# Performance work log

Measured on AMD Instinct MI355X. Metric: run time of the kernel, lower is better.

## Reference

```python
import jax, jax.numpy as jnp
import numpy as np

D_MODEL, NUM_HEADS, D_HEAD = 1024, 16, 64
B, T = 2, 2048


def setup_inputs() -> dict:
    key = jax.random.key(0)
    ks = jax.random.split(key, 9)
    s_in = 1.0 / np.sqrt(D_MODEL)
    s_proj = 1.0 / np.sqrt(NUM_HEADS * D_HEAD)
    x = jax.random.normal(ks[0], (B, T, D_MODEL), dtype=jnp.float32)
    # stacked per-head projection weights (nn.Linear: y = x @ W.T + b -> store as [H, C, d_head])
    Wq = jax.random.uniform(ks[1], (NUM_HEADS, D_MODEL, D_HEAD), jnp.float32, -s_in, s_in)
    Wk = jax.random.uniform(ks[2], (NUM_HEADS, D_MODEL, D_HEAD), jnp.float32, -s_in, s_in)
    Wv = jax.random.uniform(ks[3], (NUM_HEADS, D_MODEL, D_HEAD), jnp.float32, -s_in, s_in)
    bq = jax.random.uniform(ks[4], (NUM_HEADS, D_HEAD), jnp.float32, -s_in, s_in)
    bk = jax.random.uniform(ks[5], (NUM_HEADS, D_HEAD), jnp.float32, -s_in, s_in)
    bv = jax.random.uniform(ks[6], (NUM_HEADS, D_HEAD), jnp.float32, -s_in, s_in)
    Wo = jax.random.uniform(ks[7], (NUM_HEADS * D_HEAD, D_MODEL), jnp.float32, -s_proj, s_proj)
    bo = jax.random.uniform(ks[8], (D_MODEL,), jnp.float32, -s_proj, s_proj)
    return {"x": x, "Wq": Wq, "Wk": Wk, "Wv": Wv, "bq": bq, "bk": bk, "bv": bv, "Wo": Wo, "bo": bo}


def reference(x, Wq, Wk, Wv, bq, bk, bv, Wo, bo):
    Bsz, Tlen, C = x.shape
    # per-head projections, vectorized over heads: [B, H, T, d_head]
    q = jnp.einsum('btc,hcd->bhtd', x, Wq) + bq[None, :, None, :]
    k = jnp.einsum('btc,hcd->bhtd', x, Wk) + bk[None, :, None, :]
    v = jnp.einsum('btc,hcd->bhtd', x, Wv) + bv[None, :, None, :]
    # NOTE: source scales by sqrt(C) = sqrt(d_model), not sqrt(d_head); no causal mask
    scores = jnp.einsum('bhtd,bhsd->bhts', q, k) / jnp.sqrt(jnp.asarray(C, x.dtype))
    attn = jax.nn.softmax(scores, axis=-1)
    out = jnp.einsum('bhts,bhsd->bhtd', attn, v)  # [B, H, T, d_head]
    # concat heads along feature dim: [B, T, H*d_head]
    out = jnp.transpose(out, (0, 2, 1, 3)).reshape(Bsz, Tlen, -1)
    return out @ Wo + bo
```

## Files before the change

kernel.cpp:

```cpp
#include <hip/hip_runtime.h>

typedef __bf16 bf16;
typedef __bf16 bf16x4 __attribute__((ext_vector_type(4)));
typedef __bf16 bf16x8 __attribute__((ext_vector_type(8)));
typedef float  f32x4  __attribute__((ext_vector_type(4)));

#define T_SEQ  2048
#define NHEAD  16
#define DHEAD  64
#define DMODEL 1024
#define MTOT   4096
#define L2E    1.4426950408889634f

static __device__ __forceinline__ f32x4 mfma16(bf16x8 a, bf16x8 b, f32x4 c) {
    return __builtin_amdgcn_mfma_f32_16x16x32_bf16(a, b, c, 0, 0, 0);
}

__global__ __launch_bounds__(256) void prep(
    const float* __restrict__ x,  bf16* __restrict__ xbf,
    const float* __restrict__ Wq, const float* __restrict__ Wk,
    const float* __restrict__ Wv, bf16* __restrict__ wt,
    const float* __restrict__ Wo, bf16* __restrict__ wot)
{
    __shared__ float t[64][68];
    const int bid = blockIdx.x, tid = threadIdx.x;

    if (bid < 2048) {
        const int i = bid * 256 + tid;
        const float4 a = ((const float4*)x)[i * 2];
        const float4 b = ((const float4*)x)[i * 2 + 1];
        bf16x8 v;
        v[0] = (bf16)a.x; v[1] = (bf16)a.y; v[2] = (bf16)a.z; v[3] = (bf16)a.w;
        v[4] = (bf16)b.x; v[5] = (bf16)b.y; v[6] = (bf16)b.z; v[7] = (bf16)b.w;
        ((bf16x8*)xbf)[i] = v;
        return;
    }

    const float* in; bf16* out;
    int R, Cc; long ib, ob; int r0, c0;
    if (bid < 2816) {
        int b2 = bid - 2048;
        int w = b2 >> 8, rem = b2 & 255;
        int rt = rem & 15, head = rem >> 4;
        in  = (w == 0 ? Wq : w == 1 ? Wk : Wv);
        out = wt + (size_t)w * 1024 * 1024;
        R = 1024; Cc = 64;
        ib = (long)head * 65536; ob = (long)head * 65536;
        r0 = rt * 64; c0 = 0;
    } else {
        int b3 = bid - 2816;
        in = Wo; out = wot;
        R = 1024; Cc = 1024;
        ib = 0; ob = 0;
        r0 = (b3 & 15) * 64; c0 = (b3 >> 4) * 64;
    }

#pragma unroll
    for (int i = 0; i < 4; ++i) {
        int idx = i * 256 + tid;
        int row = idx >> 4, cb = (idx & 15) * 4;
        float4 v = *(const float4*)&in[ib + (long)(r0 + row) * Cc + c0 + cb];
        t[row][cb + 0] = v.x; t[row][cb + 1] = v.y;
        t[row][cb + 2] = v.z; t[row][cb + 3] = v.w;
    }
    __syncthreads();
#pragma unroll
    for (int i = 0; i < 2; ++i) {
        int idx = i * 256 + tid;
        int row = idx >> 3, cb = (idx & 7) * 8;
        bf16x8 v;
#pragma unroll
        for (int j = 0; j < 8; ++j) v[j] = (bf16)t[cb + j][row];
        *(bf16x8*)&out[ob + (long)(c0 + row) * R + r0 + cb] = v;
    }
}

__global__ __launch_bounds__(256) void qkv_gemm(
    const bf16* __restrict__ x, const bf16* __restrict__ wt,
    const float* __restrict__ bq, const float* __restrict__ bk,
    const float* __restrict__ bv,
    bf16* __restrict__ qws, bf16* __restrict__ kws, bf16* __restrict__ vtws)
{
    __shared__ __align__(16) bf16 xs[128][72];
    __shared__ __align__(16) bf16 wsh[3][64][72];

    const int m0 = blockIdx.x * 128;
    const int h  = blockIdx.y;
    const int tid = threadIdx.x, wid = tid >> 6, lane = tid & 63;
    const int lr = lane & 15, lg = lane >> 4;

    const bf16* wbase[3];
#pragma unroll
    for (int w = 0; w < 3; ++w)
        wbase[w] = wt + ((size_t)(w * NHEAD + h)) * DHEAD * DMODEL;

    f32x4 acc[3][2][4];
#pragma unroll
    for (int w = 0; w < 3; ++w)
#pragma unroll
        for (int mi = 0; mi < 2; ++mi)
#pragma unroll
            for (int nt = 0; nt < 4; ++nt) acc[w][mi][nt] = (f32x4)0.0f;

    bf16x8 xr[4], wr[3][2];
#pragma unroll
    for (int i = 0; i < 4; ++i) {
        int idx = i * 256 + tid;
        int row = idx >> 3, cb = (idx & 7) * 8;
        xr[i] = *(const bf16x8*)&x[(size_t)(m0 + row) * DMODEL + cb];
    }
#pragma unroll
    for (int w = 0; w < 3; ++w)
#pragma unroll
        for (int i = 0; i < 2; ++i) {
            int idx = i * 256 + tid;
            int row = idx >> 3, cb = (idx & 7) * 8;
            wr[w][i] = *(const bf16x8*)&wbase[w][(size_t)row * DMODEL + cb];
        }

    for (int kt = 0; kt < 16; ++kt) {
        __syncthreads();
#pragma unroll
        for (int i = 0; i < 4; ++i) {
            int idx = i * 256 + tid;
            int row = idx >> 3, cb = (idx & 7) * 8;
            *(bf16x8*)&xs[row][cb] = xr[i];
        }
#pragma unroll
        for (int w = 0; w < 3; ++w)
#pragma unroll
            for (int i = 0; i < 2; ++i) {
                int idx = i * 256 + tid;
                int row = idx >> 3, cb = (idx & 7) * 8;
                *(bf16x8*)&wsh[w][row][cb] = wr[w][i];
            }
        __syncthreads();

        if (kt < 15) {
            const int kofs = (kt + 1) * 64;
#pragma unroll
            for (int i = 0; i < 4; ++i) {
                int idx = i * 256 + tid;
                int row = idx >> 3, cb = (idx & 7) * 8;
                xr[i] = *(const bf16x8*)&x[(size_t)(m0 + row) * DMODEL + kofs + cb];
            }
#pragma unroll
            for (int w = 0; w < 3; ++w)
#pragma unroll
                for (int i = 0; i < 2; ++i) {
                    int idx = i * 256 + tid;
                    int row = idx >> 3, cb = (idx & 7) * 8;
                    wr[w][i] = *(const bf16x8*)&wbase[w][(size_t)row * DMODEL + kofs + cb];
                }
        }

        bf16x8 af[2][2];
#pragma unroll
        for (int mi = 0; mi < 2; ++mi)
#pragma unroll
            for (int ks = 0; ks < 2; ++ks)
                af[mi][ks] = *(const bf16x8*)&xs[wid * 32 + mi * 16 + lr][ks * 32 + lg * 8];

#pragma unroll
        for (int w = 0; w < 3; ++w)
#pragma unroll
            for (int nt = 0; nt < 4; ++nt)
#pragma unroll
                for (int ks = 0; ks < 2; ++ks) {
                    bf16x8 bfr = *(const bf16x8*)&wsh[w][nt * 16 + lr][ks * 32 + lg * 8];
#pragma unroll
                    for (int mi = 0; mi < 2; ++mi)
                        acc[w][mi][nt] = mfma16(af[mi][ks], bfr, acc[w][mi][nt]);
                }
    }

    const float* bias[3] = { bq + h * DHEAD, bk + h * DHEAD, bv + h * DHEAD };
#pragma unroll
    for (int w = 0; w < 3; ++w)
#pragma unroll
        for (int nt = 0; nt < 4; ++nt) {
            int d = nt * 16 + lr;
            float bs = bias[w][d];
#pragma unroll
            for (int mi = 0; mi < 2; ++mi)
#pragma unroll
                for (int j = 0; j < 4; ++j) {
                    int mrow = m0 + wid * 32 + mi * 16 + lg * 4 + j;
                    int b = mrow >> 11, t = mrow & 2047;
                    float val = acc[w][mi][nt][j] + bs;
                    size_t bh = (size_t)b * NHEAD + h;
                    if (w == 0)
                        qws[(bh * T_SEQ + t) * DHEAD + d] = (bf16)val;
                    else if (w == 1)
                        kws[(bh * T_SEQ + t) * DHEAD + d] = (bf16)val;
                    else
                        vtws[(bh * DHEAD + d) * T_SEQ + t] = (bf16)val;
                }
        }
}

template<int S, bool PARTIAL>
__global__ __launch_bounds__(512) void attn_split(
    const bf16* __restrict__ qws, const bf16* __restrict__ kws,
    const bf16* __restrict__ vtws,
    bf16* __restrict__ po, float* __restrict__ pml, bf16* __restrict__ aws)
{
    __shared__ __align__(16) bf16 kls[2][64][72];
    __shared__ __align__(16) bf16 vls[2][64][72];
    __shared__ __align__(16) bf16 pls[128][68];

    const int id = blockIdx.x;
    const int w  = (id & 7) * (64 * S) + (id >> 3);
    const int bh = w / (16 * S);
    const int rem = w - bh * (16 * S);
    const int qt = rem / S;
    const int sidx = rem - qt * S;
    const int t0 = (sidx * 32) / S, t1 = ((sidx + 1) * 32) / S;

    const int b = bh >> 4, h = bh & 15;
    const bf16* Q  = qws  + (size_t)bh * T_SEQ * DHEAD;
    const bf16* K  = kws  + (size_t)bh * T_SEQ * DHEAD;
    const bf16* Vt = vtws + (size_t)bh * DHEAD * T_SEQ;

    const int tid = threadIdx.x, wid = tid >> 6, lane = tid & 63;
    const int lr = lane & 15, lg = lane >> 4;
    const int q0 = qt * 128 + wid * 16;

    const int srow = tid >> 3, scb = (tid & 7) * 8;

    bf16x8 qf[2];
#pragma unroll
    for (int ks = 0; ks < 2; ++ks) {
        bf16x8 v = *(const bf16x8*)&Q[(size_t)(q0 + lr) * DHEAD + ks * 32 + lg * 8];
#pragma unroll
        for (int j = 0; j < 8; ++j) v[j] = (bf16)((float)v[j] * 0.03125f);
        qf[ks] = v;
    }

    f32x4 o[4];
#pragma unroll
    for (int nt = 0; nt < 4; ++nt) o[nt] = (f32x4)0.0f;
    float mrun = -1e30f, lrun = 0.f;

    bf16x8 kr, vr;
    kr = *(const bf16x8*)&K[(size_t)(t0 * 64 + srow) * DHEAD + scb];
    vr = *(const bf16x8*)&Vt[(size_t)srow * T_SEQ + t0 * 64 + scb];
    *(bf16x8*)&kls[0][srow][scb] = kr;
    *(bf16x8*)&vls[0][srow][scb] = vr;

    int cur = 0;
    for (int t = t0; t < t1; ++t) {
        __syncthreads();

        const bool more = (t + 1) < t1;
        if (more) {
            int kvn = (t + 1) * 64;
            kr = *(const bf16x8*)&K[(size_t)(kvn + srow) * DHEAD + scb];
            vr = *(const bf16x8*)&Vt[(size_t)srow * T_SEQ + kvn + scb];
        }

        f32x4 s[4];
        __builtin_amdgcn_s_setprio(1);
#pragma unroll
        for (int nt = 0; nt < 4; ++nt) {
            bf16x8 k0 = *(const bf16x8*)&kls[cur][nt * 16 + lr][0 + lg * 8];
            bf16x8 k1 = *(const bf16x8*)&kls[cur][nt * 16 + lr][32 + lg * 8];
            s[nt] = mfma16(k0, qf[0], (f32x4)0.0f);
            s[nt] = mfma16(k1, qf[1], s[nt]);
        }
        __builtin_amdgcn_s_setprio(0);

        float vm0 = fmaxf(fmaxf(s[0][0], s[0][1]), fmaxf(s[0][2], s[0][3]));
        float vm1 = fmaxf(fmaxf(s[1][0], s[1][1]), fmaxf(s[1][2], s[1][3]));
        float vm2 = fmaxf(fmaxf(s[2][0], s[2][1]), fmaxf(s[2][2], s[2][3]));
        float vm3 = fmaxf(fmaxf(s[3][0], s[3][1]), fmaxf(s[3][2], s[3][3]));
        float vm = fmaxf(fmaxf(vm0, vm1), fmaxf(vm2, vm3));
        vm = fmaxf(vm, __shfl_xor(vm, 16));
        vm = fmaxf(vm, __shfl_xor(vm, 32));

        const bool skip = __all(vm <= mrun + 8.0f);
        float mnew = skip ? mrun : fmaxf(mrun, vm);
        float m2 = mnew * L2E;

        float p[4][4];
        float rs = 0.f;
#pragma unroll
        for (int nt = 0; nt < 4; ++nt)
#pragma unroll
            for (int j = 0; j < 4; ++j) {
                p[nt][j] = __builtin_amdgcn_exp2f(fmaf(s[nt][j], L2E, -m2));
                rs += p[nt][j];
            }

        if (skip) {
            lrun += rs;
        } else {
            float alpha = __builtin_amdgcn_exp2f((mrun - mnew) * L2E);
            lrun = lrun * alpha + rs;
            mrun = mnew;
            float ab[4];
#pragma unroll
            for (int j = 0; j < 4; ++j) ab[j] = __shfl(alpha, lg * 4 + j);
#pragma unroll
            for (int nt = 0; nt < 4; ++nt)
#pragma unroll
                for (int j = 0; j < 4; ++j) o[nt][j] *= ab[j];
        }

#pragma unroll
        for (int nt = 0; nt < 4; ++nt) {
            bf16x4 pk;
            pk[0] = (bf16)p[nt][0]; pk[1] = (bf16)p[nt][1];
            pk[2] = (bf16)p[nt][2]; pk[3] = (bf16)p[nt][3];
            *(bf16x4*)&pls[wid * 16 + lr][nt * 16 + 4 * lg] = pk;
        }

        asm volatile("s_waitcnt lgkmcnt(0)" ::: "memory");

        __builtin_amdgcn_s_setprio(1);
#pragma unroll
        for (int ks = 0; ks < 2; ++ks) {
            bf16x4 ph0 = *(const bf16x4*)&pls[wid * 16 + lr][ks * 32 + lg * 8];
            bf16x4 ph1 = *(const bf16x4*)&pls[wid * 16 + lr][ks * 32 + lg * 8 + 4];
            bf16x8 pf = __builtin_shufflevector(ph0, ph1, 0, 1, 2, 3, 4, 5, 6, 7);
#pragma unroll
            for (int nt = 0; nt < 4; ++nt) {
                bf16x8 vf = *(const bf16x8*)&vls[cur][nt * 16 + lr][ks * 32 + lg * 8];
                o[nt] = mfma16(pf, vf, o[nt]);
            }
        }
        __builtin_amdgcn_s_setprio(0);

        if (more) {
            *(bf16x8*)&kls[cur ^ 1][srow][scb] = kr;
            *(bf16x8*)&vls[cur ^ 1][srow][scb] = vr;
        }
        cur ^= 1;
    }

    float lrow = lrun;
    lrow += __shfl_xor(lrow, 16);
    lrow += __shfl_xor(lrow, 32);

    float linv[4];
#pragma unroll
    for (int j = 0; j < 4; ++j) linv[j] = 1.0f / __shfl(lrow, lg * 4 + j);

    if (PARTIAL) {
        const size_t pbase = (size_t)(sidx * 32 + bh) * T_SEQ * DHEAD;
#pragma unroll
        for (int nt = 0; nt < 4; ++nt) {
            int d = nt * 16 + lr;
#pragma unroll
            for (int j = 0; j < 4; ++j) {
                int tq = q0 + lg * 4 + j;
                po[pbase + (size_t)tq * DHEAD + d] = (bf16)(o[nt][j] * linv[j]);
            }
        }
        if (lg == 0) {
            size_t mlidx = ((size_t)(sidx * 32 + bh) * T_SEQ + (q0 + lr)) * 2;
            pml[mlidx]     = mrun;
            pml[mlidx + 1] = lrow;
        }
    } else {
        const size_t obase = ((size_t)b * T_SEQ) * DMODEL + (size_t)h * DHEAD;
#pragma unroll
        for (int nt = 0; nt < 4; ++nt) {
            int d = nt * 16 + lr;
#pragma unroll
            for (int j = 0; j < 4; ++j) {
                int tq = q0 + lg * 4 + j;
                aws[obase + (size_t)tq * DMODEL + d] = (bf16)(o[nt][j] * linv[j]);
            }
        }
    }
}

template<int S>
__global__ __launch_bounds__(256) void attn_combine(
    const bf16* __restrict__ po, const float* __restrict__ pml,
    bf16* __restrict__ aws)
{
    const int g = blockIdx.x * 256 + threadIdx.x;
    const int r = g >> 3, dblk = g & 7;
    const int bh = r >> 11, tq = r & 2047;

    float ms[S], ls[S];
    float m = -1e30f;
#pragma unroll
    for (int s = 0; s < S; ++s) {
        float2 v = ((const float2*)pml)[(size_t)(s * 32 + bh) * T_SEQ + tq];
        ms[s] = v.x; ls[s] = v.y;
        m = fmaxf(m, ms[s]);
    }
    float L = 0.f, wgt[S];
#pragma unroll
    for (int s = 0; s < S; ++s) {
        wgt[s] = ls[s] * __builtin_amdgcn_exp2f((ms[s] - m) * L2E);
        L += wgt[s];
    }
    float inv = 1.0f / L;

    float acc[8];
#pragma unroll
    for (int j = 0; j < 8; ++j) acc[j] = 0.f;
#pragma unroll
    for (int s = 0; s < S; ++s) {
        bf16x8 ov = *(const bf16x8*)&po[((size_t)(s * 32 + bh) * T_SEQ + tq) * DHEAD + dblk * 8];
        float c = wgt[s] * inv;
#pragma unroll
        for (int j = 0; j < 8; ++j) acc[j] = fmaf(c, (float)ov[j], acc[j]);
    }
    bf16x8 out;
#pragma unroll
    for (int j = 0; j < 8; ++j) out[j] = (bf16)acc[j];

    const int b = bh >> 4, h = bh & 15;
    *(bf16x8*)&aws[((size_t)(b * T_SEQ + tq)) * DMODEL + h * DHEAD + dblk * 8] = out;
}

__global__ __launch_bounds__(256) void out_gemm(
    const bf16* __restrict__ a, const bf16* __restrict__ wot,
    const float* __restrict__ bo, float* __restrict__ out)
{
    __shared__ __align__(16) bf16 as[128][72];
    __shared__ __align__(16) bf16 wsh[128][72];

    const int m0 = blockIdx.x * 128, n0 = blockIdx.y * 128;
    const int tid = threadIdx.x, wid = tid >> 6, lane = tid & 63;
    const int lr = lane & 15, lg = lane >> 4;

    f32x4 acc[2][8];
#pragma unroll
    for (int mi = 0; mi < 2; ++mi)
#pragma unroll
        for (int nt = 0; nt < 8; ++nt) acc[mi][nt] = (f32x4)0.0f;

    bf16x8 ar[4], wr[4];
#pragma unroll
    for (int i = 0; i < 4; ++i) {
        int idx = i * 256 + tid;
        int row = idx >> 3, cb = (idx & 7) * 8;
        ar[i] = *(const bf16x8*)&a[(size_t)(m0 + row) * DMODEL + cb];
        wr[i] = *(const bf16x8*)&wot[(size_t)(n0 + row) * DMODEL + cb];
    }

    for (int kt = 0; kt < 16; ++kt) {
        __syncthreads();
#pragma unroll
        for (int i = 0; i < 4; ++i) {
            int idx = i * 256 + tid;
            int row = idx >> 3, cb = (idx & 7) * 8;
            *(bf16x8*)&as[row][cb]  = ar[i];
            *(bf16x8*)&wsh[row][cb] = wr[i];
        }
        __syncthreads();

        if (kt < 15) {
            const int kofs = (kt + 1) * 64;
#pragma unroll
            for (int i = 0; i < 4; ++i) {
                int idx = i * 256 + tid;
                int row = idx >> 3, cb = (idx & 7) * 8;
                ar[i] = *(const bf16x8*)&a[(size_t)(m0 + row) * DMODEL + kofs + cb];
                wr[i] = *(const bf16x8*)&wot[(size_t)(n0 + row) * DMODEL + kofs + cb];
            }
        }

        bf16x8 af[2][2];
#pragma unroll
        for (int mi = 0; mi < 2; ++mi)
#pragma unroll
            for (int ks = 0; ks < 2; ++ks)
                af[mi][ks] = *(const bf16x8*)&as[wid * 32 + mi * 16 + lr][ks * 32 + lg * 8];

#pragma unroll
        for (int nt = 0; nt < 8; ++nt)
#pragma unroll
            for (int ks = 0; ks < 2; ++ks) {
                bf16x8 bfr = *(const bf16x8*)&wsh[nt * 16 + lr][ks * 32 + lg * 8];
#pragma unroll
                for (int mi = 0; mi < 2; ++mi)
                    acc[mi][nt] = mfma16(af[mi][ks], bfr, acc[mi][nt]);
            }
    }

#pragma unroll
    for (int nt = 0; nt < 8; ++nt) {
        int n = n0 + nt * 16 + lr;
        float bs = bo[n];
#pragma unroll
        for (int mi = 0; mi < 2; ++mi)
#pragma unroll
            for (int j = 0; j < 4; ++j) {
                int m = m0 + wid * 32 + mi * 16 + lg * 4 + j;
                out[(size_t)m * DMODEL + n] = acc[mi][nt][j] + bs;
            }
    }
}

extern "C" void kernel_launch(void* const* d_in, const int* in_sizes, int n_in,
                              void* d_out, int out_size, void* d_ws, size_t ws_size,
                              hipStream_t stream)
{
    const float* x  = (const float*)d_in[0];
    const float* Wq = (const float*)d_in[1];
    const float* Wk = (const float*)d_in[2];
    const float* Wv = (const float*)d_in[3];
    const float* bq = (const float*)d_in[4];
    const float* bk = (const float*)d_in[5];
    const float* bv = (const float*)d_in[6];
    const float* Wo = (const float*)d_in[7];
    const float* bo = (const float*)d_in[8];
    float* out = (float*)d_out;

    const size_t M1 = (size_t)1024 * 1024;
    bf16* ws   = (bf16*)d_ws;
    bf16* xbf  = ws;
    bf16* qws  = ws + 4 * M1;
    bf16* kws  = qws + 4 * M1;
    bf16* vtws = kws + 4 * M1;
    bf16* wt   = vtws + 4 * M1;
    bf16* wot  = wt + 3 * M1;
    bf16* aws  = xbf;
    bf16* po   = wot + 1 * M1;

    const size_t BASE = 20 * M1 * 2;
    const size_t PER  = 4 * M1 * 2 + (size_t)65536 * 2 * 4;

    dim3 tb(256);
    prep<<<dim3(3072), tb, 0, stream>>>(x, xbf, Wq, Wk, Wv, wt, Wo, wot);
    qkv_gemm<<<dim3(MTOT / 128, NHEAD), tb, 0, stream>>>(xbf, wt, bq, bk, bv, qws, kws, vtws);

    if (ws_size >= BASE + 3 * PER) {
        float* pml = (float*)(po + 3 * 4 * M1);
        attn_split<3, true><<<dim3(1536), dim3(512), 0, stream>>>(qws, kws, vtws, po, pml, aws);
        attn_combine<3><<<dim3(2048), tb, 0, stream>>>(po, pml, aws);
    } else if (ws_size >= BASE + 2 * PER) {
        float* pml = (float*)(po + 2 * 4 * M1);
        attn_split<2, true><<<dim3(1024), dim3(512), 0, stream>>>(qws, kws, vtws, po, pml, aws);
        attn_combine<2><<<dim3(2048), tb, 0, stream>>>(po, pml, aws);
    } else {
        attn_split<1, false><<<dim3(512), dim3(512), 0, stream>>>(qws, kws, vtws, po, nullptr, aws);
    }

    out_gemm<<<dim3(MTOT / 128, DMODEL / 128), tb, 0, stream>>>(aws, wot, bo, out);
}
```

Baseline: 135.9 us.

## Use 1024-thread attention blocks with 256-query tiles and split K/V loading

Doubles the attention block to 16 waves covering 256 query rows, so each K/V tile staged in shared memory is reused by twice as many queries. Loading is split so half the threads fetch K and half fetch V, which halves the per-thread global loads and the register buffering. The 3-way KV split path is dropped and the largest path becomes a 2-way split with 512 blocks. The risk is fewer blocks, which means less latency hiding and possible CU underutilisation. The launch-bounds change to (1024, 8) may also constrain registers.

```diff
diff --git a/kernel.cpp b/kernel.cpp
--- a/kernel.cpp
+++ b/kernel.cpp
@@ -200,19 +200,19 @@
 }
 
 template<int S, bool PARTIAL>
-__global__ __launch_bounds__(512) void attn_split(
+__global__ __launch_bounds__(1024, 8) void attn_split(
     const bf16* __restrict__ qws, const bf16* __restrict__ kws,
     const bf16* __restrict__ vtws,
     bf16* __restrict__ po, float* __restrict__ pml, bf16* __restrict__ aws)
 {
     __shared__ __align__(16) bf16 kls[2][64][72];
     __shared__ __align__(16) bf16 vls[2][64][72];
-    __shared__ __align__(16) bf16 pls[128][68];
+    __shared__ __align__(16) bf16 pls[256][68];
 
     const int id = blockIdx.x;
-    const int w  = (id & 7) * (64 * S) + (id >> 3);
-    const int bh = w / (16 * S);
-    const int rem = w - bh * (16 * S);
+    const int w  = (id & 7) * (32 * S) + (id >> 3);
+    const int bh = w / (8 * S);
+    const int rem = w - bh * (8 * S);
     const int qt = rem / S;
     const int sidx = rem - qt * S;
     const int t0 = (sidx * 32) / S, t1 = ((sidx + 1) * 32) / S;
@@ -224,9 +224,10 @@
 
     const int tid = threadIdx.x, wid = tid >> 6, lane = tid & 63;
     const int lr = lane & 15, lg = lane >> 4;
-    const int q0 = qt * 128 + wid * 16;
-
-    const int srow = tid >> 3, scb = (tid & 7) * 8;
+    const int q0 = qt * 256 + wid * 16;
+
+    const bool kpart = tid < 512;
+    const int srow = (tid >> 3) & 63, scb = (tid & 7) * 8;
 
     bf16x8 qf[2];
 #pragma unroll
@@ -242,11 +243,11 @@
     for (int nt = 0; nt < 4; ++nt) o[nt] = (f32x4)0.0f;
     float mrun = -1e30f, lrun = 0.f;
 
-    bf16x8 kr, vr;
-    kr = *(const bf16x8*)&K[(size_t)(t0 * 64 + srow) * DHEAD + scb];
-    vr = *(const bf16x8*)&Vt[(size_t)srow * T_SEQ + t0 * 64 + scb];
-    *(bf16x8*)&kls[0][srow][scb] = kr;
-    *(bf16x8*)&vls[0][srow][scb] = vr;
+    bf16x8 r;
+    if (kpart) r = *(const bf16x8*)&K[(size_t)(t0 * 64 + srow) * DHEAD + scb];
+    else       r = *(const bf16x8*)&Vt[(size_t)srow * T_SEQ + t0 * 64 + scb];
+    if (kpart) *(bf16x8*)&kls[0][srow][scb] = r;
+    else       *(bf16x8*)&vls[0][srow][scb] = r;
 
     int cur = 0;
     for (int t = t0; t < t1; ++t) {
@@ -255,8 +256,8 @@
         const bool more = (t + 1) < t1;
         if (more) {
             int kvn = (t + 1) * 64;
-            kr = *(const bf16x8*)&K[(size_t)(kvn + srow) * DHEAD + scb];
-            vr = *(const bf16x8*)&Vt[(size_t)srow * T_SEQ + kvn + scb];
+            if (kpart) r = *(const bf16x8*)&K[(size_t)(kvn + srow) * DHEAD + scb];
+            else       r = *(const bf16x8*)&Vt[(size_t)srow * T_SEQ + kvn + scb];
         }
 
         f32x4 s[4];
@@ -332,8 +333,8 @@
         __builtin_amdgcn_s_setprio(0);
 
         if (more) {
-            *(bf16x8*)&kls[cur ^ 1][srow][scb] = kr;
-            *(bf16x8*)&vls[cur ^ 1][srow][scb] = vr;
+            if (kpart) *(bf16x8*)&kls[cur ^ 1][srow][scb] = r;
+            else       *(bf16x8*)&vls[cur ^ 1][srow][scb] = r;
         }
         cur ^= 1;
     }
@@ -350,11 +351,11 @@
         const size_t pbase = (size_t)(sidx * 32 + bh) * T_SEQ * DHEAD;
 #pragma unroll
         for (int nt = 0; nt < 4; ++nt) {
-            int d = nt * 16 + lr;
+            int dcol = nt * 16 + lr;
 #pragma unroll
             for (int j = 0; j < 4; ++j) {
                 int tq = q0 + lg * 4 + j;
-                po[pbase + (size_t)tq * DHEAD + d] = (bf16)(o[nt][j] * linv[j]);
+                po[pbase + (size_t)tq * DHEAD + dcol] = (bf16)(o[nt][j] * linv[j]);
             }
         }
         if (lg == 0) {
@@ -366,11 +367,11 @@
         const size_t obase = ((size_t)b * T_SEQ) * DMODEL + (size_t)h * DHEAD;
 #pragma unroll
         for (int nt = 0; nt < 4; ++nt) {
-            int d = nt * 16 + lr;
+            int dcol = nt * 16 + lr;
 #pragma unroll
             for (int j = 0; j < 4; ++j) {
                 int tq = q0 + lg * 4 + j;
-                aws[obase + (size_t)tq * DMODEL + d] = (bf16)(o[nt][j] * linv[j]);
+                aws[obase + (size_t)tq * DMODEL + dcol] = (bf16)(o[nt][j] * linv[j]);
             }
         }
     }
@@ -532,16 +533,12 @@
     prep<<<dim3(3072), tb, 0, stream>>>(x, xbf, Wq, Wk, Wv, wt, Wo, wot);
     qkv_gemm<<<dim3(MTOT / 128, NHEAD), tb, 0, stream>>>(xbf, wt, bq, bk, bv, qws, kws, vtws);
 
-    if (ws_size >= BASE + 3 * PER) {
-        float* pml = (float*)(po + 3 * 4 * M1);
-        attn_split<3, true><<<dim3(1536), dim3(512), 0, stream>>>(qws, kws, vtws, po, pml, aws);
-        attn_combine<3><<<dim3(2048), tb, 0, stream>>>(po, pml, aws);
-    } else if (ws_size >= BASE + 2 * PER) {
+    if (ws_size >= BASE + 2 * PER) {
         float* pml = (float*)(po + 2 * 4 * M1);
-        attn_split<2, true><<<dim3(1024), dim3(512), 0, stream>>>(qws, kws, vtws, po, pml, aws);
+        attn_split<2, true><<<dim3(512), dim3(1024), 0, stream>>>(qws, kws, vtws, po, pml, aws);
         attn_combine<2><<<dim3(2048), tb, 0, stream>>>(po, pml, aws);
     } else {
-        attn_split<1, false><<<dim3(512), dim3(512), 0, stream>>>(qws, kws, vtws, po, nullptr, aws);
+        attn_split<1, false><<<dim3(256), dim3(1024), 0, stream>>>(qws, kws, vtws, po, nullptr, aws);
     }
 
     out_gemm<<<dim3(MTOT / 128, DMODEL / 128), tb, 0, stream>>>(aws, wot, bo, out);
```

After: 141.0 us. 3.7% more time.

## Process two query groups per attention block to reuse K/V tiles

Applied to the files above, without the earlier changes.

Each attention workgroup now handles 256 query rows (two 128-row groups per wave) instead of 128. Every K/V tile loaded into shared memory therefore feeds twice as many MFMAs, halving K/V global and LDS traffic per query. The 3-way KV split path is dropped, so a large workspace now falls to the 2-way split with half as many blocks. The trade-off is higher register pressure (launch bounds of 512 threads with a minimum of 4 blocks), a larger P buffer in shared memory, and fewer blocks to fill the GPU.

```diff
diff --git a/kernel.cpp b/kernel.cpp
--- a/kernel.cpp
+++ b/kernel.cpp
@@ -200,19 +200,19 @@
 }
 
 template<int S, bool PARTIAL>
-__global__ __launch_bounds__(512) void attn_split(
+__global__ __launch_bounds__(512, 4) void attn_split(
     const bf16* __restrict__ qws, const bf16* __restrict__ kws,
     const bf16* __restrict__ vtws,
     bf16* __restrict__ po, float* __restrict__ pml, bf16* __restrict__ aws)
 {
     __shared__ __align__(16) bf16 kls[2][64][72];
     __shared__ __align__(16) bf16 vls[2][64][72];
-    __shared__ __align__(16) bf16 pls[128][68];
+    __shared__ __align__(16) bf16 pls[256][68];
 
     const int id = blockIdx.x;
-    const int w  = (id & 7) * (64 * S) + (id >> 3);
-    const int bh = w / (16 * S);
-    const int rem = w - bh * (16 * S);
+    const int w  = (id & 7) * (32 * S) + (id >> 3);
+    const int bh = w / (8 * S);
+    const int rem = w - bh * (8 * S);
     const int qt = rem / S;
     const int sidx = rem - qt * S;
     const int t0 = (sidx * 32) / S, t1 = ((sidx + 1) * 32) / S;
@@ -224,23 +224,29 @@
 
     const int tid = threadIdx.x, wid = tid >> 6, lane = tid & 63;
     const int lr = lane & 15, lg = lane >> 4;
-    const int q0 = qt * 128 + wid * 16;
 
     const int srow = tid >> 3, scb = (tid & 7) * 8;
 
-    bf16x8 qf[2];
-#pragma unroll
-    for (int ks = 0; ks < 2; ++ks) {
-        bf16x8 v = *(const bf16x8*)&Q[(size_t)(q0 + lr) * DHEAD + ks * 32 + lg * 8];
-#pragma unroll
-        for (int j = 0; j < 8; ++j) v[j] = (bf16)((float)v[j] * 0.03125f);
-        qf[ks] = v;
-    }
-
-    f32x4 o[4];
-#pragma unroll
-    for (int nt = 0; nt < 4; ++nt) o[nt] = (f32x4)0.0f;
-    float mrun = -1e30f, lrun = 0.f;
+    int q0[2];
+    bf16x8 qf[2][2];
+#pragma unroll
+    for (int g = 0; g < 2; ++g) {
+        q0[g] = qt * 256 + g * 128 + wid * 16;
+#pragma unroll
+        for (int ks = 0; ks < 2; ++ks) {
+            bf16x8 v = *(const bf16x8*)&Q[(size_t)(q0[g] + lr) * DHEAD + ks * 32 + lg * 8];
+#pragma unroll
+            for (int j = 0; j < 8; ++j) v[j] = (bf16)((float)v[j] * 0.03125f);
+            qf[g][ks] = v;
+        }
+    }
+
+    f32x4 o[2][4];
+#pragma unroll
+    for (int g = 0; g < 2; ++g)
+#pragma unroll
+        for (int nt = 0; nt < 4; ++nt) o[g][nt] = (f32x4)0.0f;
+    float mrun[2] = { -1e30f, -1e30f }, lrun[2] = { 0.f, 0.f };
 
     bf16x8 kr, vr;
     kr = *(const bf16x8*)&K[(size_t)(t0 * 64 + srow) * DHEAD + scb];
@@ -259,60 +265,66 @@
             vr = *(const bf16x8*)&Vt[(size_t)srow * T_SEQ + kvn + scb];
         }
 
-        f32x4 s[4];
+        f32x4 s[2][4];
         __builtin_amdgcn_s_setprio(1);
 #pragma unroll
         for (int nt = 0; nt < 4; ++nt) {
             bf16x8 k0 = *(const bf16x8*)&kls[cur][nt * 16 + lr][0 + lg * 8];
             bf16x8 k1 = *(const bf16x8*)&kls[cur][nt * 16 + lr][32 + lg * 8];
-            s[nt] = mfma16(k0, qf[0], (f32x4)0.0f);
-            s[nt] = mfma16(k1, qf[1], s[nt]);
+#pragma unroll
+            for (int g = 0; g < 2; ++g) {
+                s[g][nt] = mfma16(k0, qf[g][0], (f32x4)0.0f);
+                s[g][nt] = mfma16(k1, qf[g][1], s[g][nt]);
+            }
         }
         __builtin_amdgcn_s_setprio(0);
 
-        float vm0 = fmaxf(fmaxf(s[0][0], s[0][1]), fmaxf(s[0][2], s[0][3]));
-        float vm1 = fmaxf(fmaxf(s[1][0], s[1][1]), fmaxf(s[1][2], s[1][3]));
-        float vm2 = fmaxf(fmaxf(s[2][0], s[2][1]), fmaxf(s[2][2], s[2][3]));
-        float vm3 = fmaxf(fmaxf(s[3][0], s[3][1]), fmaxf(s[3][2], s[3][3]));
-        float vm = fmaxf(fmaxf(vm0, vm1), fmaxf(vm2, vm3));
-        vm = fmaxf(vm, __shfl_xor(vm, 16));
-        vm = fmaxf(vm, __shfl_xor(vm, 32));
-
-        const bool skip = __all(vm <= mrun + 8.0f);
-        float mnew = skip ? mrun : fmaxf(mrun, vm);
-        float m2 = mnew * L2E;
-
-        float p[4][4];
-        float rs = 0.f;
-#pragma unroll
-        for (int nt = 0; nt < 4; ++nt)
-#pragma unroll
-            for (int j = 0; j < 4; ++j) {
-                p[nt][j] = __builtin_amdgcn_exp2f(fmaf(s[nt][j], L2E, -m2));
-                rs += p[nt][j];
-            }
-
-        if (skip) {
-            lrun += rs;
-        } else {
-            float alpha = __builtin_amdgcn_exp2f((mrun - mnew) * L2E);
-            lrun = lrun * alpha + rs;
-            mrun = mnew;
-            float ab[4];
-#pragma unroll
-            for (int j = 0; j < 4; ++j) ab[j] = __shfl(alpha, lg * 4 + j);
+#pragma unroll
+        for (int g = 0; g < 2; ++g) {
+            float vm0 = fmaxf(fmaxf(s[g][0][0], s[g][0][1]), fmaxf(s[g][0][2], s[g][0][3]));
+            float vm1 = fmaxf(fmaxf(s[g][1][0], s[g][1][1]), fmaxf(s[g][1][2], s[g][1][3]));
+            float vm2 = fmaxf(fmaxf(s[g][2][0], s[g][2][1]), fmaxf(s[g][2][2], s[g][2][3]));
+            float vm3 = fmaxf(fmaxf(s[g][3][0], s[g][3][1]), fmaxf(s[g][3][2], s[g][3][3]));
+            float vm = fmaxf(fmaxf(vm0, vm1), fmaxf(vm2, vm3));
+            vm = fmaxf(vm, __shfl_xor(vm, 16));
+            vm = fmaxf(vm, __shfl_xor(vm, 32));
+
+            const bool skip = __all(vm <= mrun[g] + 8.0f);
+            float mnew = skip ? mrun[g] : fmaxf(mrun[g], vm);
+            float m2 = mnew * L2E;
+
+            float p[4][4];
+            float rs = 0.f;
 #pragma unroll
             for (int nt = 0; nt < 4; ++nt)
 #pragma unroll
-                for (int j = 0; j < 4; ++j) o[nt][j] *= ab[j];
-        }
-
-#pragma unroll
-        for (int nt = 0; nt < 4; ++nt) {
-            bf16x4 pk;
-            pk[0] = (bf16)p[nt][0]; pk[1] = (bf16)p[nt][1];
-            pk[2] = (bf16)p[nt][2]; pk[3] = (bf16)p[nt][3];
-            *(bf16x4*)&pls[wid * 16 + lr][nt * 16 + 4 * lg] = pk;
+                for (int j = 0; j < 4; ++j) {
+                    p[nt][j] = __builtin_amdgcn_exp2f(fmaf(s[g][nt][j], L2E, -m2));
+                    rs += p[nt][j];
+                }
+
+            if (skip) {
+                lrun[g] += rs;
+            } else {
+                float alpha = __builtin_amdgcn_exp2f((mrun[g] - mnew) * L2E);
+                lrun[g] = lrun[g] * alpha + rs;
+                mrun[g] = mnew;
+                float ab[4];
+#pragma unroll
+                for (int j = 0; j < 4; ++j) ab[j] = __shfl(alpha, lg * 4 + j);
+#pragma unroll
+                for (int nt = 0; nt < 4; ++nt)
+#pragma unroll
+                    for (int j = 0; j < 4; ++j) o[g][nt][j] *= ab[j];
+            }
+
+#pragma unroll
+            for (int nt = 0; nt < 4; ++nt) {
+                bf16x4 pk;
+                pk[0] = (bf16)p[nt][0]; pk[1] = (bf16)p[nt][1];
+                pk[2] = (bf16)p[nt][2]; pk[3] = (bf16)p[nt][3];
+                *(bf16x4*)&pls[g * 128 + wid * 16 + lr][nt * 16 + 4 * lg] = pk;
+            }
         }
 
         asm volatile("s_waitcnt lgkmcnt(0)" ::: "memory");
@@ -320,13 +332,19 @@
         __builtin_amdgcn_s_setprio(1);
 #pragma unroll
         for (int ks = 0; ks < 2; ++ks) {
-            bf16x4 ph0 = *(const bf16x4*)&pls[wid * 16 + lr][ks * 32 + lg * 8];
-            bf16x4 ph1 = *(const bf16x4*)&pls[wid * 16 + lr][ks * 32 + lg * 8 + 4];
-            bf16x8 pf = __builtin_shufflevector(ph0, ph1, 0, 1, 2, 3, 4, 5, 6, 7);
+            bf16x8 pf[2];
+#pragma unroll
+            for (int g = 0; g < 2; ++g) {
+                bf16x4 ph0 = *(const bf16x4*)&pls[g * 128 + wid * 16 + lr][ks * 32 + lg * 8];
+                bf16x4 ph1 = *(const bf16x4*)&pls[g * 128 + wid * 16 + lr][ks * 32 + lg * 8 + 4];
+                pf[g] = __builtin_shufflevector(ph0, ph1, 0, 1, 2, 3, 4, 5, 6, 7);
+            }
 #pragma unroll
             for (int nt = 0; nt < 4; ++nt) {
                 bf16x8 vf = *(const bf16x8*)&vls[cur][nt * 16 + lr][ks * 32 + lg * 8];
-                o[nt] = mfma16(pf, vf, o[nt]);
+#pragma unroll
+                for (int g = 0; g < 2; ++g)
+                    o[g][nt] = mfma16(pf[g], vf, o[g][nt]);
             }
         }
         __builtin_amdgcn_s_setprio(0);
@@ -338,39 +356,42 @@
         cur ^= 1;
     }
 
-    float lrow = lrun;
-    lrow += __shfl_xor(lrow, 16);
-    lrow += __shfl_xor(lrow, 32);
-
-    float linv[4];
-#pragma unroll
-    for (int j = 0; j < 4; ++j) linv[j] = 1.0f / __shfl(lrow, lg * 4 + j);
-
-    if (PARTIAL) {
-        const size_t pbase = (size_t)(sidx * 32 + bh) * T_SEQ * DHEAD;
-#pragma unroll
-        for (int nt = 0; nt < 4; ++nt) {
-            int d = nt * 16 + lr;
-#pragma unroll
-            for (int j = 0; j < 4; ++j) {
-                int tq = q0 + lg * 4 + j;
-                po[pbase + (size_t)tq * DHEAD + d] = (bf16)(o[nt][j] * linv[j]);
-            }
-        }
-        if (lg == 0) {
-            size_t mlidx = ((size_t)(sidx * 32 + bh) * T_SEQ + (q0 + lr)) * 2;
-            pml[mlidx]     = mrun;
-            pml[mlidx + 1] = lrow;
-        }
-    } else {
-        const size_t obase = ((size_t)b * T_SEQ) * DMODEL + (size_t)h * DHEAD;
-#pragma unroll
-        for (int nt = 0; nt < 4; ++nt) {
-            int d = nt * 16 + lr;
-#pragma unroll
-            for (int j = 0; j < 4; ++j) {
-                int tq = q0 + lg * 4 + j;
-                aws[obase + (size_t)tq * DMODEL + d] = (bf16)(o[nt][j] * linv[j]);
+#pragma unroll
+    for (int g = 0; g < 2; ++g) {
+        float lrow = lrun[g];
+        lrow += __shfl_xor(lrow, 16);
+        lrow += __shfl_xor(lrow, 32);
+
+        float linv[4];
+#pragma unroll
+        for (int j = 0; j < 4; ++j) linv[j] = 1.0f / __shfl(lrow, lg * 4 + j);
+
+        if (PARTIAL) {
+            const size_t pbase = (size_t)(sidx * 32 + bh) * T_SEQ * DHEAD;
+#pragma unroll
+            for (int nt = 0; nt < 4; ++nt) {
+                int dcol = nt * 16 + lr;
+#pragma unroll
+                for (int j = 0; j < 4; ++j) {
+                    int tq = q0[g] + lg * 4 + j;
+                    po[pbase + (size_t)tq * DHEAD + dcol] = (bf16)(o[g][nt][j] * linv[j]);
+                }
+            }
+            if (lg == 0) {
+                size_t mlidx = ((size_t)(sidx * 32 + bh) * T_SEQ + (q0[g] + lr)) * 2;
+                pml[mlidx]     = mrun[g];
+                pml[mlidx + 1] = lrow;
+            }
+        } else {
+            const size_t obase = ((size_t)b * T_SEQ) * DMODEL + (size_t)h * DHEAD;
+#pragma unroll
+            for (int nt = 0; nt < 4; ++nt) {
+                int dcol = nt * 16 + lr;
+#pragma unroll
+                for (int j = 0; j < 4; ++j) {
+                    int tq = q0[g] + lg * 4 + j;
+                    aws[obase + (size_t)tq * DMODEL + dcol] = (bf16)(o[g][nt][j] * linv[j]);
+                }
             }
         }
     }
@@ -532,16 +553,12 @@
     prep<<<dim3(3072), tb, 0, stream>>>(x, xbf, Wq, Wk, Wv, wt, Wo, wot);
     qkv_gemm<<<dim3(MTOT / 128, NHEAD), tb, 0, stream>>>(xbf, wt, bq, bk, bv, qws, kws, vtws);
 
-    if (ws_size >= BASE + 3 * PER) {
-        float* pml = (float*)(po + 3 * 4 * M1);
-        attn_split<3, true><<<dim3(1536), dim3(512), 0, stream>>>(qws, kws, vtws, po, pml, aws);
-        attn_combine<3><<<dim3(2048), tb, 0, stream>>>(po, pml, aws);
-    } else if (ws_size >= BASE + 2 * PER) {
+    if (ws_size >= BASE + 2 * PER) {
         float* pml = (float*)(po + 2 * 4 * M1);
-        attn_split<2, true><<<dim3(1024), dim3(512), 0, stream>>>(qws, kws, vtws, po, pml, aws);
+        attn_split<2, true><<<dim3(512), dim3(512), 0, stream>>>(qws, kws, vtws, po, pml, aws);
         attn_combine<2><<<dim3(2048), tb, 0, stream>>>(po, pml, aws);
     } else {
-        attn_split<1, false><<<dim3(512), dim3(512), 0, stream>>>(qws, kws, vtws, po, nullptr, aws);
+        attn_split<1, false><<<dim3(256), dim3(512), 0, stream>>>(qws, kws, vtws, po, nullptr, aws);
     }
 
     out_gemm<<<dim3(MTOT / 128, DMODEL / 128), tb, 0, stream>>>(aws, wot, bo, out);
```

New measurement: 126.4 us. -7.0%, faster.
